# Performance work log

Hardware: AMD Instinct MI355X
Metric: run time of the kernel (lower is better)

## Reference

```python
import jax, jax.numpy as jnp
import numpy as np

# Fixed hierarchical grouping of the 15 regions into 5 groups of 3 (from split_regions)
SPLIT_IDX = np.array([[0, 1, 8], [2, 4, 6], [3, 5, 7], [9, 11, 13], [10, 12, 14]])
BN_EPS = 1e-5


def _bn_relu(x, g, b):
    # BatchNorm over (batch, spatial) dims in training-stats mode, then ReLU
    mu = jnp.mean(x, axis=(0, 2, 3), keepdims=True)
    var = jnp.var(x, axis=(0, 2, 3), keepdims=True)
    xn = (x - mu) * jax.lax.rsqrt(var + BN_EPS)
    return jax.nn.relu(xn * g[None, :, None, None] + b[None, :, None, None])


def _local_agg(x, params):
    # x: [B, Cin, G, K]; pointwise conv (1x1) -> BN -> ReLU per layer, then max over K
    for W, g, b in params:
        x = jnp.einsum('oi,bigk->bogk', W, x)
        x = _bn_relu(x, g, b)
    return jnp.max(x, axis=-1)  # [B, Cout, G]


def setup_inputs() -> dict:
    key = jax.random.key(0)
    ks = jax.random.split(key, 8)
    B, G, K = 32, 15, 2048
    inp = {"local_regions": jax.random.normal(ks[0], (B, G, K, 3), jnp.float32)}
    chans = [(3, 64, 64), (67, 128, 128), (131, 256, 256)]
    ki = 1
    for li, (c0, c1, c2) in enumerate(chans):
        for wi, (co, ci) in enumerate([(c1, c0), (c2, c1)]):
            inp[f"la{li}_w{wi}"] = jax.random.normal(ks[ki], (co, ci), jnp.float32) * (1.0 / np.sqrt(ci))
            inp[f"la{li}_g{wi}"] = jnp.ones((co,), jnp.float32)
            inp[f"la{li}_b{wi}"] = jnp.zeros((co,), jnp.float32)
            ki += 1
    return inp


def reference(local_regions,
              la0_w0, la0_g0, la0_b0, la0_w1, la0_g1, la0_b1,
              la1_w0, la1_g0, la1_b0, la1_w1, la1_g1, la1_b1,
              la2_w0, la2_g0, la2_b0, la2_w1, la2_g1, la2_b1):
    la0 = [(la0_w0, la0_g0, la0_b0), (la0_w1, la0_g1, la0_b1)]
    la1 = [(la1_w0, la1_g0, la1_b0), (la1_w1, la1_g1, la1_b1)]
    la2 = [(la2_w0, la2_g0, la2_b0), (la2_w1, la2_g1, la2_b1)]
    idx = jnp.asarray(SPLIT_IDX)

    x = jnp.transpose(local_regions, (0, 3, 1, 2))  # [B, 3, 15, K]
    centroids_1 = jnp.mean(x, axis=-1)              # [B, 3, 15]
    relative_1 = x - centroids_1[..., None]
    lf1 = _local_agg(relative_1, la0)               # [B, 64, 15]
    local_features = jnp.concatenate([centroids_1, lf1], axis=1)  # [B, 67, 15]

    # level 2: regroup 15 regions into [5, 3]
    lf1_s = jnp.transpose(lf1, (0, 2, 1))[:, idx, :]         # [B, 5, 3, 64]
    lr2 = jnp.transpose(centroids_1, (0, 2, 1))[:, idx, :]   # [B, 5, 3, 3]
    c2 = jnp.mean(lr2, axis=2)                               # [B, 5, 3]
    rel2 = lr2 - c2[:, :, None, :]
    feats2 = jnp.concatenate([rel2, lf1_s], axis=-1)         # [B, 5, 3, 67]
    feats2 = jnp.transpose(feats2, (0, 3, 1, 2))             # [B, 67, 5, 3]
    lf2 = _local_agg(feats2, la1)                            # [B, 128, 5]

    # level 3: global
    c3 = jnp.mean(c2, axis=1)                                # [B, 3]
    rel3 = c2 - c3[:, None, :]                               # [B, 5, 3]
    lf2 = jnp.concatenate([jnp.transpose(rel3, (0, 2, 1)), lf2], axis=1)  # [B, 131, 5]
    lf2 = lf2[:, :, None, :]                                 # [B, 131, 1, 5]
    gf = _local_agg(lf2, la2)                                # [B, 256, 1]
    return gf.squeeze(2), local_features
```

## Files before the change

### kernel.cpp

```cpp
#include <hip/hip_runtime.h>
#include <math.h>

#define BB 32
#define GG 15
#define KK 2048
#define NB 480
#define N1F 983040.0f
#define EPS 1e-5f
#define PZN ((int)0xAAAAAAAA)

typedef _Float16 half8 __attribute__((ext_vector_type(8)));
typedef float f32x4 __attribute__((ext_vector_type(4)));

#define WS_CENT  0
#define WS_H2B   1920
#define WS_H3B   63360
#define GSREL    104320
#define GBN1     104560
#define G2A      108400
#define G2B      116080
#define G3A      123760
#define G3B      128880
#define CNT_GRP  134000
#define CNT_SUP  134192
#define CNT_DONE 134198

#define SMEMF 7936

__device__ const int SIDX[15] = {0,1,8, 2,4,6, 3,5,7, 9,11,13, 10,12,14};
__device__ const int INV[15]  = {0,1,3,6,4,7,5,8,2,9,12,10,13,11,14};

__device__ __forceinline__ float wave_sum(float v){
    for (int off = 32; off; off >>= 1) v += __shfl_down(v, off, 64);
    return v;
}
__device__ __forceinline__ float aloadf(const float* p){
    return __hip_atomic_load(p, __ATOMIC_RELAXED, __HIP_MEMORY_SCOPE_AGENT);
}
__device__ __forceinline__ int aloadi(const int* p){
    return __hip_atomic_load(p, __ATOMIC_RELAXED, __HIP_MEMORY_SCOPE_AGENT);
}
template<int SLP>
__device__ __forceinline__ void gbar(int* wsi, int idx, int gi, int ngrp){
    __syncthreads();
    if (threadIdx.x == 0) {
        if (atomicAdd(&wsi[CNT_GRP + idx*32 + gi], 1) == PZN + 15) {
            if (atomicAdd(&wsi[CNT_SUP + idx], 1) == PZN + ngrp - 1)
                atomicExch(&wsi[CNT_DONE + idx], 1);
        }
        int g = 0;
        while (aloadi(&wsi[CNT_DONE + idx]) != 1 && ++g < 4000000)
            __builtin_amdgcn_s_sleep(SLP);
    }
    __syncthreads();
    asm volatile("" ::: "memory");
}

__global__ void __launch_bounds__(256, 2) mega(
        const float* __restrict__ x,
        const float* __restrict__ w00, const float* __restrict__ g00, const float* __restrict__ b00,
        const float* __restrict__ w01, const float* __restrict__ g01, const float* __restrict__ b01,
        const float* __restrict__ w10, const float* __restrict__ g10, const float* __restrict__ b10,
        const float* __restrict__ w11, const float* __restrict__ g11, const float* __restrict__ b11,
        const float* __restrict__ w20, const float* __restrict__ g20, const float* __restrict__ b20,
        const float* __restrict__ w21, const float* __restrict__ g21, const float* __restrict__ b21,
        float* __restrict__ ws, float* __restrict__ out) {
    __shared__ __align__(16) float smemf[SMEMF];
    float* xls  = smemf;
    float* redM = smemf + 6144; float* redN = smemf + 6400;
    float* redS = smemf + 6656; float* redQ = smemf + 6912;
    float* bcast= smemf + 7168;
    float* c2ls = smemf + 7184; float* c3ls = smemf + 7200;
    float* f2ls = smemf + 7204;
    float* vA   = smemf + 7272;
    float* f3ls = smemf + 7400;
    float* h3ls = smemf + 7532;
    int* wsi = (int*)ws;

    int bid = blockIdx.x, tid = threadIdx.x;
    int b_ = bid / GG, g_ = bid % GG;
    int wv = tid >> 6, lane = tid & 63, l15 = lane & 15, quad = lane >> 4;
    int gi = bid >> 4;

    {
        const float4* xp4 = (const float4*)(x + (size_t)bid * KK * 3);
        float4* xls4 = (float4*)xls;
        #pragma unroll
        for (int i = 0; i < 6; i++) xls4[i*256 + tid] = xp4[i*256 + tid];
        __syncthreads();
        float m[9] = {0,0,0,0,0,0,0,0,0};
        float a[24];
        const float* bp = &xls[tid*24];
        #pragma unroll
        for (int i = 0; i < 6; i++)
            *reinterpret_cast<float4*>(&a[i*4]) = *reinterpret_cast<const float4*>(&bp[i*4]);
        #pragma unroll
        for (int p = 0; p < 8; p++) {
            float ax=a[p*3], ay=a[p*3+1], az=a[p*3+2];
            m[0]+=ax; m[1]+=ay; m[2]+=az;
            m[3]=fmaf(ax,ax,m[3]); m[4]=fmaf(ay,ay,m[4]); m[5]=fmaf(az,az,m[5]);
            m[6]=fmaf(ax,ay,m[6]); m[7]=fmaf(ax,az,m[7]); m[8]=fmaf(ay,az,m[8]);
        }
        #pragma unroll
        for (int q = 0; q < 9; q++) {
            float v = wave_sum(m[q]);
            if (lane == 0) redM[q*4 + wv] = v;
        }
        __syncthreads();
        if (tid == 0) {
            float t[9];
            #pragma unroll
            for (int q = 0; q < 9; q++) t[q] = redM[q*4]+redM[q*4+1]+redM[q*4+2]+redM[q*4+3];
            float c0 = t[0]/KK, c1 = t[1]/KK, c2 = t[2]/KK;
            bcast[0]=c0; bcast[1]=c1; bcast[2]=c2;
            out[8192 + b_*(67*GG) + 0*GG + g_] = c0;
            out[8192 + b_*(67*GG) + 1*GG + g_] = c1;
            out[8192 + b_*(67*GG) + 2*GG + g_] = c2;
            atomicExch(&ws[WS_CENT + bid*4 + 0], c0);
            atomicExch(&ws[WS_CENT + bid*4 + 1], c1);
            atomicExch(&ws[WS_CENT + bid*4 + 2], c2);
            redM[40] = t[3] - KK*c0*c0;  redM[41] = t[4] - KK*c1*c1;
            redM[42] = t[5] - KK*c2*c2;  redM[43] = t[6] - KK*c0*c1;
            redM[44] = t[7] - KK*c0*c2;  redM[45] = t[8] - KK*c1*c2;
        }
        __syncthreads();
    }
    if (tid < 6) atomicAdd(&ws[GSREL + gi*8 + tid], redM[40 + tid]);

    half8 afA[4], afB[4];
    #pragma unroll
    for (int t = 0; t < 4; t++)
        #pragma unroll
        for (int j = 0; j < 8; j++) {
            afA[t][j] = (_Float16)w01[(t*16 + l15)*64 + quad*8 + j];
            afB[t][j] = (_Float16)w01[(t*16 + l15)*64 + 32 + quad*8 + j];
        }
    gbar<8>(wsi, 0, gi, 30);

    if (tid < 6) {
        float acc = 0.f;
        #pragma unroll
        for (int s = 0; s < 30; s++) acc += aloadf(&ws[GSREL + s*8 + tid]);
        bcast[3+tid] = acc / N1F;
    }
    if (tid >= 64 && tid < 79) {
        int t2 = tid-64, s = t2/3, i = t2%3;
        float acc = 0.f;
        #pragma unroll
        for (int j = 0; j < 3; j++)
            acc += aloadf(&ws[WS_CENT + (b_*GG + SIDX[s*3+j])*4 + i]);
        c2ls[t2] = acc * (1.f/3.f);
    }
    __syncthreads();
    if (tid < 3) {
        float a = 0.f;
        for (int s = 0; s < 5; s++) a += c2ls[s*3+tid];
        c3ls[tid] = a * 0.2f;
    }
    __syncthreads();
    float c0 = bcast[0], c1 = bcast[1], c2v = bcast[2];
    float S00=bcast[3], S11=bcast[4], S22=bcast[5], S01=bcast[6], S02=bcast[7], S12=bcast[8];

    float wa0[8], wa1[8], wa2[8], ba[8], wb0[8], wb1[8], wb2[8], bb[8];
    #pragma unroll
    for (int j = 0; j < 8; j++) {
        int cA = quad*8 + j;
        float u0=w00[cA*3+0], u1=w00[cA*3+1], u2=w00[cA*3+2];
        float var = u0*u0*S00 + u1*u1*S11 + u2*u2*S22
                  + 2.f*(u0*u1*S01 + u0*u2*S02 + u1*u2*S12);
        float a1 = g00[cA]*rsqrtf(var + EPS);
        wa0[j]=a1*u0; wa1[j]=a1*u1; wa2[j]=a1*u2; ba[j]=b00[cA];
        int cB = cA + 32;
        float v0=w00[cB*3+0], v1=w00[cB*3+1], v2=w00[cB*3+2];
        float varB = v0*v0*S00 + v1*v1*S11 + v2*v2*S22
                   + 2.f*(v0*v1*S01 + v0*v2*S02 + v1*v2*S12);
        float a1B = g00[cB]*rsqrtf(varB + EPS);
        wb0[j]=a1B*v0; wb1[j]=a1B*v1; wb2[j]=a1B*v2; bb[j]=b00[cB];
    }
    float mx[16], mn[16], sm[16], sq[16];
    #pragma unroll
    for (int s = 0; s < 16; s++) { mx[s]=-1e30f; mn[s]=1e30f; sm[s]=0.f; sq[s]=0.f; }

    for (int it = 0; it < 32; it++) {
        int k = it*64 + wv*16 + l15;
        float r0 = xls[k*3+0]-c0, r1 = xls[k*3+1]-c1, r2 = xls[k*3+2]-c2v;
        half8 bf0, bf1;
        #pragma unroll
        for (int j = 0; j < 8; j++) {
            float pA = fmaf(wa0[j],r0, fmaf(wa1[j],r1, fmaf(wa2[j],r2, ba[j])));
            bf0[j] = (_Float16)fmaxf(pA, 0.f);
            float pB = fmaf(wb0[j],r0, fmaf(wb1[j],r1, fmaf(wb2[j],r2, bb[j])));
            bf1[j] = (_Float16)fmaxf(pB, 0.f);
        }
        #pragma unroll
        for (int t = 0; t < 4; t++) {
            f32x4 acc = {0.f,0.f,0.f,0.f};
            acc = __builtin_amdgcn_mfma_f32_16x16x32_f16(afA[t], bf0, acc, 0, 0, 0);
            acc = __builtin_amdgcn_mfma_f32_16x16x32_f16(afB[t], bf1, acc, 0, 0, 0);
            #pragma unroll
            for (int r = 0; r < 4; r++) {
                float h = acc[r];
                int s = t*4 + r;
                mx[s]=fmaxf(mx[s],h); mn[s]=fminf(mn[s],h);
                sm[s]+=h;             sq[s]=fmaf(h,h,sq[s]);
            }
        }
    }
    #pragma unroll
    for (int m = 1; m < 16; m <<= 1) {
        #pragma unroll
        for (int s = 0; s < 16; s++) {
            mx[s] = fmaxf(mx[s], __shfl_xor(mx[s], m, 64));
            mn[s] = fminf(mn[s], __shfl_xor(mn[s], m, 64));
            sm[s] += __shfl_xor(sm[s], m, 64);
            sq[s] += __shfl_xor(sq[s], m, 64);
        }
    }
    __syncthreads();
    if (l15 == 0) {
        #pragma unroll
        for (int t = 0; t < 4; t++)
            #pragma unroll
            for (int r = 0; r < 4; r++) {
                int o = t*16 + quad*4 + r;
                redM[wv*64+o]=mx[t*4+r]; redN[wv*64+o]=mn[t*4+r];
                redS[wv*64+o]=sm[t*4+r]; redQ[wv*64+o]=sq[t*4+r];
            }
    }
    __syncthreads();
    float Mreg = -1e30f, Nreg = 1e30f;
    if (tid < 64) {
        float S=0.f, Q=0.f;
        #pragma unroll
        for (int w = 0; w < 4; w++) {
            Mreg = fmaxf(Mreg, redM[w*64+tid]); Nreg = fminf(Nreg, redN[w*64+tid]);
            S += redS[w*64+tid];               Q += redQ[w*64+tid];
        }
        atomicAdd(&ws[GBN1 + gi*128 + tid], S);
        atomicAdd(&ws[GBN1 + gi*128 + 64 + tid], Q);
    }
    gbar<8>(wsi, 1, gi, 30);

    int p_ = INV[g_];

    if (tid < 64) {
        float SM = 0.f, SQ = 0.f;
        #pragma unroll
        for (int s = 0; s < 30; s++) {
            SM += aloadf(&ws[GBN1 + s*128 + tid]);
            SQ += aloadf(&ws[GBN1 + s*128 + 64 + tid]);
        }
        float mean = SM / N1F;
        float var  = SQ / N1F - mean*mean;
        float s1 = g01[tid]*rsqrtf(var + EPS);
        float t1 = b01[tid] - mean*s1;
        float val = fmaxf(fmaf(s1, (s1 >= 0.f) ? Mreg : Nreg, t1), 0.f);
        f2ls[3+tid] = val;
        out[8192 + b_*(67*GG) + (3+tid)*GG + g_] = val;
    } else if (tid < 67) {
        int i = tid - 64;
        f2ls[i] = bcast[i] - c2ls[(p_/3)*3 + i];
    }
    __syncthreads();

    if (tid < 128) {
        const float* wr = w10 + tid*67;
        float h = 0.f;
        #pragma unroll
        for (int c = 0; c < 67; c++) h = fmaf(wr[c], f2ls[c], h);
        vA[tid] = h;
        atomicAdd(&ws[G2A + gi*256 + tid], h);
        atomicAdd(&ws[G2A + gi*256 + 128 + tid], h*h);
    }
    gbar<4>(wsi, 2, gi, 30);

    {
        int o = tid & 127, ph = tid >> 7;
        if (tid < 128) {
            float SM = 0.f, SQ = 0.f;
            #pragma unroll
            for (int s = 0; s < 30; s++) {
                SM += aloadf(&ws[G2A + s*256 + tid]);
                SQ += aloadf(&ws[G2A + s*256 + 128 + tid]);
            }
            float mean = SM/480.f, var = SQ/480.f - mean*mean;
            float s2 = g10[tid]*rsqrtf(var+EPS), t2 = b10[tid] - mean*s2;
            vA[tid] = fmaxf(fmaf(s2, vA[tid], t2), 0.f);
        }
        __syncthreads();
        const float* wr = w11 + o*128 + ph*64;
        const float* vv = vA + ph*64;
        float hacc = 0.f;
        #pragma unroll
        for (int j = 0; j < 64; j++) hacc = fmaf(wr[j], vv[j], hacc);
        redM[tid] = hacc;
        __syncthreads();
        if (tid < 128) {
            float h = redM[tid] + redM[tid+128];
            atomicExch(&ws[WS_H2B + (b_*GG + p_)*128 + tid], h);
            atomicAdd(&ws[G2B + gi*256 + tid], h);
            atomicAdd(&ws[G2B + gi*256 + 128 + tid], h*h);
        }
    }
    gbar<4>(wsi, 3, gi, 30);
    if (g_ >= 5) return;

    int pi = b_*5 + g_;
    int gi2 = pi >> 4;

    {
        int s5 = g_;
        if (tid < 128) {
            float SM = 0.f, SQ = 0.f;
            #pragma unroll
            for (int s = 0; s < 30; s++) {
                SM += aloadf(&ws[G2B + s*256 + tid]);
                SQ += aloadf(&ws[G2B + s*256 + 128 + tid]);
            }
            float mean = SM/480.f, var = SQ/480.f - mean*mean;
            float s3 = g11[tid]*rsqrtf(var+EPS), t3 = b11[tid] - mean*s3;
            float m = -1e30f;
            #pragma unroll
            for (int j = 0; j < 3; j++) {
                float hv = aloadf(&ws[WS_H2B + (b_*GG + s5*3 + j)*128 + tid]);
                m = fmaxf(m, fmaxf(fmaf(s3, hv, t3), 0.f));
            }
            f3ls[3+tid] = m;
        } else if (tid < 131) {
            int i = tid - 128;
            f3ls[i] = c2ls[s5*3+i] - c3ls[i];
        }
        __syncthreads();
        const float* wr = w20 + tid*131;
        float hacc = 0.f;
        #pragma unroll 4
        for (int c = 0; c < 131; c++) hacc = fmaf(wr[c], f3ls[c], hacc);
        h3ls[tid] = hacc;
        atomicAdd(&ws[G3A + gi2*512 + tid], hacc);
        atomicAdd(&ws[G3A + gi2*512 + 256 + tid], hacc*hacc);
    }
    gbar<4>(wsi, 4, gi2, 10);

    {
        float SM = 0.f, SQ = 0.f;
        #pragma unroll
        for (int s = 0; s < 10; s++) {
            SM += aloadf(&ws[G3A + s*512 + tid]);
            SQ += aloadf(&ws[G3A + s*512 + 256 + tid]);
        }
        float mean = SM/160.f, var = SQ/160.f - mean*mean;
        float s4 = g20[tid]*rsqrtf(var+EPS), t4 = b20[tid] - mean*s4;
        h3ls[tid] = fmaxf(fmaf(s4, h3ls[tid], t4), 0.f);
        __syncthreads();
        const float* wr = w21 + tid*256;
        float hacc = 0.f;
        #pragma unroll 4
        for (int i = 0; i < 256; i++) hacc = fmaf(wr[i], h3ls[i], hacc);
        atomicExch(&ws[WS_H3B + pi*256 + tid], hacc);
        atomicAdd(&ws[G3B + gi2*512 + tid], hacc);
        atomicAdd(&ws[G3B + gi2*512 + 256 + tid], hacc*hacc);
    }
    gbar<4>(wsi, 5, gi2, 10);
    if (g_ != 0) return;

    {
        float SM = 0.f, SQ = 0.f;
        #pragma unroll
        for (int s = 0; s < 10; s++) {
            SM += aloadf(&ws[G3B + s*512 + tid]);
            SQ += aloadf(&ws[G3B + s*512 + 256 + tid]);
        }
        float mean = SM/160.f, var = SQ/160.f - mean*mean;
        float s5c = g21[tid]*rsqrtf(var+EPS), t5 = b21[tid] - mean*s5c;
        float m = -1e30f;
        #pragma unroll
        for (int jj = 0; jj < 5; jj++) {
            float hv = aloadf(&ws[WS_H3B + (b_*5 + jj)*256 + tid]);
            m = fmaxf(m, fmaxf(fmaf(s5c, hv, t5), 0.f));
        }
        out[b_*256 + tid] = m;
    }
}

extern "C" void kernel_launch(void* const* d_in, const int* in_sizes, int n_in,
                              void* d_out, int out_size, void* d_ws, size_t ws_size,
                              hipStream_t stream) {
    (void)in_sizes; (void)n_in; (void)out_size; (void)ws_size;
    const float* x   = (const float*)d_in[0];
    const float* w00 = (const float*)d_in[1];
    const float* g00 = (const float*)d_in[2];
    const float* b00 = (const float*)d_in[3];
    const float* w01 = (const float*)d_in[4];
    const float* g01 = (const float*)d_in[5];
    const float* b01 = (const float*)d_in[6];
    const float* w10 = (const float*)d_in[7];
    const float* g10 = (const float*)d_in[8];
    const float* b10 = (const float*)d_in[9];
    const float* w11 = (const float*)d_in[10];
    const float* g11 = (const float*)d_in[11];
    const float* b11 = (const float*)d_in[12];
    const float* w20 = (const float*)d_in[13];
    const float* g20 = (const float*)d_in[14];
    const float* b20 = (const float*)d_in[15];
    const float* w21 = (const float*)d_in[16];
    const float* g21 = (const float*)d_in[17];
    const float* b21 = (const float*)d_in[18];
    float* out = (float*)d_out;
    float* ws  = (float*)d_ws;

    mega<<<NB, 256, 0, stream>>>(x, w00,g00,b00, w01,g01,b01, w10,g10,b10,
                                 w11,g11,b11, w20,g20,b20, w21,g21,b21, ws, out);
}
```

Before: 202.9 us.

## Fold partial BN statistics once in last-arriving block before barrier release

The last block to reach each grid barrier now sums the per-group partial statistics and writes the totals to new workspace slots before releasing the barrier. Every other block then reads a single precomputed value instead of each re-summing 30 or 10 partials with atomic loads. This trims redundant global atomic traffic after every barrier. In exchange, the reduction now sits on the barrier's critical path, and each barrier gains extra __syncthreads and a shared flag. The workspace counter offsets also move, so the zero-init pattern has to cover the new layout.

```diff
diff --git a/kernel.cpp b/kernel.cpp
--- a/kernel.cpp
+++ b/kernel.cpp
@@ -21,9 +21,15 @@
 #define G2B      116080
 #define G3A      123760
 #define G3B      128880
-#define CNT_GRP  134000
-#define CNT_SUP  134192
-#define CNT_DONE 134198
+#define FSREL    134000
+#define FBN1     134008
+#define F2A      134136
+#define F2B      134392
+#define F3A      134648
+#define F3B      135160
+#define CNT_GRP  135672
+#define CNT_SUP  135864
+#define CNT_DONE 135870
 
 #define SMEMF 7936
 
@@ -40,14 +46,24 @@
 __device__ __forceinline__ int aloadi(const int* p){
     return __hip_atomic_load(p, __ATOMIC_RELAXED, __HIP_MEMORY_SCOPE_AGENT);
 }
-template<int SLP>
-__device__ __forceinline__ void gbar(int* wsi, int idx, int gi, int ngrp){
-    __syncthreads();
+template<int SLP, class Fold>
+__device__ __forceinline__ void gbar(int* wsi, int idx, int gi, int ngrp,
+                                     int* sflag, Fold fold){
+    __syncthreads();
+    if (threadIdx.x == 0)
+        sflag[0] = (atomicAdd(&wsi[CNT_GRP + idx*32 + gi], 1) == PZN + 15) ? 1 : 0;
+    __syncthreads();
+    if (sflag[0]) {
+        if (threadIdx.x == 0)
+            sflag[1] = (atomicAdd(&wsi[CNT_SUP + idx], 1) == PZN + ngrp - 1) ? 1 : 0;
+        __syncthreads();
+        if (sflag[1]) {
+            fold();
+            __syncthreads();
+            if (threadIdx.x == 0) atomicExch(&wsi[CNT_DONE + idx], 1);
+        }
+    }
     if (threadIdx.x == 0) {
-        if (atomicAdd(&wsi[CNT_GRP + idx*32 + gi], 1) == PZN + 15) {
-            if (atomicAdd(&wsi[CNT_SUP + idx], 1) == PZN + ngrp - 1)
-                atomicExch(&wsi[CNT_DONE + idx], 1);
-        }
         int g = 0;
         while (aloadi(&wsi[CNT_DONE + idx]) != 1 && ++g < 4000000)
             __builtin_amdgcn_s_sleep(SLP);
@@ -75,6 +91,7 @@
     float* vA   = smemf + 7272;
     float* f3ls = smemf + 7400;
     float* h3ls = smemf + 7532;
+    int*   sflag= (int*)(smemf + 7916);
     int* wsi = (int*)ws;
 
     int bid = blockIdx.x, tid = threadIdx.x;
@@ -135,14 +152,16 @@
             afA[t][j] = (_Float16)w01[(t*16 + l15)*64 + quad*8 + j];
             afB[t][j] = (_Float16)w01[(t*16 + l15)*64 + 32 + quad*8 + j];
         }
-    gbar<8>(wsi, 0, gi, 30);
-
-    if (tid < 6) {
-        float acc = 0.f;
-        #pragma unroll
-        for (int s = 0; s < 30; s++) acc += aloadf(&ws[GSREL + s*8 + tid]);
-        bcast[3+tid] = acc / N1F;
-    }
+    gbar<8>(wsi, 0, gi, 30, sflag, [&]{
+        if (tid < 6) {
+            float acc = 0.f;
+            #pragma unroll
+            for (int s = 0; s < 30; s++) acc += aloadf(&ws[GSREL + s*8 + tid]);
+            atomicExch(&ws[FSREL + tid], acc);
+        }
+    });
+
+    if (tid < 6) bcast[3+tid] = aloadf(&ws[FSREL + tid]) / N1F;
     if (tid >= 64 && tid < 79) {
         int t2 = tid-64, s = t2/3, i = t2%3;
         float acc = 0.f;
@@ -239,17 +258,20 @@
         atomicAdd(&ws[GBN1 + gi*128 + tid], S);
         atomicAdd(&ws[GBN1 + gi*128 + 64 + tid], Q);
     }
-    gbar<8>(wsi, 1, gi, 30);
+    gbar<8>(wsi, 1, gi, 30, sflag, [&]{
+        if (tid < 128) {
+            float acc = 0.f;
+            #pragma unroll
+            for (int s = 0; s < 30; s++) acc += aloadf(&ws[GBN1 + s*128 + tid]);
+            atomicExch(&ws[FBN1 + tid], acc);
+        }
+    });
 
     int p_ = INV[g_];
 
     if (tid < 64) {
-        float SM = 0.f, SQ = 0.f;
-        #pragma unroll
-        for (int s = 0; s < 30; s++) {
-            SM += aloadf(&ws[GBN1 + s*128 + tid]);
-            SQ += aloadf(&ws[GBN1 + s*128 + 64 + tid]);
-        }
+        float SM = aloadf(&ws[FBN1 + tid]);
+        float SQ = aloadf(&ws[FBN1 + 64 + tid]);
         float mean = SM / N1F;
         float var  = SQ / N1F - mean*mean;
         float s1 = g01[tid]*rsqrtf(var + EPS);
@@ -272,18 +294,18 @@
         atomicAdd(&ws[G2A + gi*256 + tid], h);
         atomicAdd(&ws[G2A + gi*256 + 128 + tid], h*h);
     }
-    gbar<4>(wsi, 2, gi, 30);
+    gbar<4>(wsi, 2, gi, 30, sflag, [&]{
+        float acc = 0.f;
+        #pragma unroll
+        for (int s = 0; s < 30; s++) acc += aloadf(&ws[G2A + s*256 + tid]);
+        atomicExch(&ws[F2A + tid], acc);
+    });
 
     {
         int o = tid & 127, ph = tid >> 7;
         if (tid < 128) {
-            float SM = 0.f, SQ = 0.f;
-            #pragma unroll
-            for (int s = 0; s < 30; s++) {
-                SM += aloadf(&ws[G2A + s*256 + tid]);
-                SQ += aloadf(&ws[G2A + s*256 + 128 + tid]);
-            }
-            float mean = SM/480.f, var = SQ/480.f - mean*mean;
+            float mean = aloadf(&ws[F2A + tid]) / 480.f;
+            float var  = aloadf(&ws[F2A + 128 + tid]) / 480.f - mean*mean;
             float s2 = g10[tid]*rsqrtf(var+EPS), t2 = b10[tid] - mean*s2;
             vA[tid] = fmaxf(fmaf(s2, vA[tid], t2), 0.f);
         }
@@ -302,7 +324,12 @@
             atomicAdd(&ws[G2B + gi*256 + 128 + tid], h*h);
         }
     }
-    gbar<4>(wsi, 3, gi, 30);
+    gbar<4>(wsi, 3, gi, 30, sflag, [&]{
+        float acc = 0.f;
+        #pragma unroll
+        for (int s = 0; s < 30; s++) acc += aloadf(&ws[G2B + s*256 + tid]);
+        atomicExch(&ws[F2B + tid], acc);
+    });
     if (g_ >= 5) return;
 
     int pi = b_*5 + g_;
@@ -311,13 +338,8 @@
     {
         int s5 = g_;
         if (tid < 128) {
-            float SM = 0.f, SQ = 0.f;
-            #pragma unroll
-            for (int s = 0; s < 30; s++) {
-                SM += aloadf(&ws[G2B + s*256 + tid]);
-                SQ += aloadf(&ws[G2B + s*256 + 128 + tid]);
-            }
-            float mean = SM/480.f, var = SQ/480.f - mean*mean;
+            float mean = aloadf(&ws[F2B + tid]) / 480.f;
+            float var  = aloadf(&ws[F2B + 128 + tid]) / 480.f - mean*mean;
             float s3 = g11[tid]*rsqrtf(var+EPS), t3 = b11[tid] - mean*s3;
             float m = -1e30f;
             #pragma unroll
@@ -339,16 +361,20 @@
         atomicAdd(&ws[G3A + gi2*512 + tid], hacc);
         atomicAdd(&ws[G3A + gi2*512 + 256 + tid], hacc*hacc);
     }
-    gbar<4>(wsi, 4, gi2, 10);
+    gbar<4>(wsi, 4, gi2, 10, sflag, [&]{
+        float a0 = 0.f, a1 = 0.f;
+        #pragma unroll
+        for (int s = 0; s < 10; s++) {
+            a0 += aloadf(&ws[G3A + s*512 + tid]);
+            a1 += aloadf(&ws[G3A + s*512 + 256 + tid]);
+        }
+        atomicExch(&ws[F3A + tid], a0);
+        atomicExch(&ws[F3A + 256 + tid], a1);
+    });
 
     {
-        float SM = 0.f, SQ = 0.f;
-        #pragma unroll
-        for (int s = 0; s < 10; s++) {
-            SM += aloadf(&ws[G3A + s*512 + tid]);
-            SQ += aloadf(&ws[G3A + s*512 + 256 + tid]);
-        }
-        float mean = SM/160.f, var = SQ/160.f - mean*mean;
+        float mean = aloadf(&ws[F3A + tid]) / 160.f;
+        float var  = aloadf(&ws[F3A + 256 + tid]) / 160.f - mean*mean;
         float s4 = g20[tid]*rsqrtf(var+EPS), t4 = b20[tid] - mean*s4;
         h3ls[tid] = fmaxf(fmaf(s4, h3ls[tid], t4), 0.f);
         __syncthreads();
@@ -360,16 +386,21 @@
         atomicAdd(&ws[G3B + gi2*512 + tid], hacc);
         atomicAdd(&ws[G3B + gi2*512 + 256 + tid], hacc*hacc);
     }
-    gbar<4>(wsi, 5, gi2, 10);
+    gbar<4>(wsi, 5, gi2, 10, sflag, [&]{
+        float a0 = 0.f, a1 = 0.f;
+        #pragma unroll
+        for (int s = 0; s < 10; s++) {
+            a0 += aloadf(&ws[G3B + s*512 + tid]);
+            a1 += aloadf(&ws[G3B + s*512 + 256 + tid]);
+        }
+        atomicExch(&ws[F3B + tid], a0);
+        atomicExch(&ws[F3B + 256 + tid], a1);
+    });
     if (g_ != 0) return;
 
     {
-        float SM = 0.f, SQ = 0.f;
-        #pragma unroll
-        for (int s = 0; s < 10; s++) {
-            SM += aloadf(&ws[G3B + s*512 + tid]);
-            SQ += aloadf(&ws[G3B + s*512 + 256 + tid]);
-        }
+        float SM = aloadf(&ws[F3B + tid]);
+        float SQ = aloadf(&ws[F3B + 256 + tid]);
         float mean = SM/160.f, var = SQ/160.f - mean*mean;
         float s5c = g21[tid]*rsqrtf(var+EPS), t5 = b21[tid] - mean*s5c;
         float m = -1e30f;
```

After: 193.0 us. 4.9% less time.
